# Kernel tuning notes

Measured on AMD Instinct MI355X. Metric: run time of the kernel, lower is better.

The kernel has to match this reference:

```python
import jax, jax.numpy as jnp
import numpy as np

N_CELL, N_GENE, D, E = 100000, 20000, 128, 1000000


def setup_inputs() -> dict:
    key = jax.random.key(0)
    ks = jax.random.split(key, 16)
    return {
        "cell_z": jax.random.normal(ks[0], (N_CELL, D), jnp.float32),
        "gene_z": jax.random.normal(ks[1], (N_GENE, D), jnp.float32),
        "W_gene": jax.random.normal(ks[2], (D, D), jnp.float32) / np.sqrt(D),
        "b_gene": jax.random.normal(ks[3], (D,), jnp.float32) * 0.01,
        "cell_scale": jax.random.normal(ks[4], (N_CELL,), jnp.float32),
        "cell_bias": jax.random.normal(ks[5], (N_CELL,), jnp.float32),
        "cell_std": jax.random.uniform(ks[6], (N_CELL,), jnp.float32, 0.1, 1.0),
        "gene_scale": jax.random.normal(ks[7], (N_GENE,), jnp.float32),
        "gene_bias": jax.random.normal(ks[8], (N_GENE,), jnp.float32),
        "gene_std": jax.random.uniform(ks[9], (N_GENE,), jnp.float32, 0.1, 1.0),
        "src_idx": jax.random.randint(ks[10], (E,), 0, N_CELL, jnp.int32),
        "dst_idx": jax.random.randint(ks[11], (E,), 0, N_GENE, jnp.int32),
        "cell_n_id": jax.random.randint(ks[12], (N_CELL,), 0, N_CELL, jnp.int32),
        "gene_n_id": jax.random.randint(ks[13], (N_GENE,), 0, N_GENE, jnp.int32),
    }


def reference(cell_z, gene_z, W_gene, b_gene,
              cell_scale, cell_bias, cell_std,
              gene_scale, gene_bias, gene_std,
              src_idx, dst_idx, cell_n_id, gene_n_id):
    # Relation projection: 'cell' -> Identity, 'gene' -> Linear + LeakyReLU.
    # Project per-node then gather (mathematically identical to the original
    # gather-then-project since projection is pointwise per node).
    gene_proj = jax.nn.leaky_relu(gene_z @ W_gene + b_gene)  # [N_GENE, D]
    u = cell_z[src_idx]            # [E, D] gather of src node embeddings
    v = gene_proj[dst_idx]         # [E, D] gather of projected dst embeddings

    # Per-edge scale/bias/std lookups via global node ids (n_id[edge_index]).
    sid = cell_n_id[src_idx]       # [E]
    did = gene_n_id[dst_idx]       # [E]
    s_sc, s_b, s_sd = cell_scale[sid], cell_bias[sid], cell_std[sid]
    d_sc, d_b, d_sd = gene_scale[did], gene_bias[did], gene_std[did]

    dot = jnp.sum(u * v, axis=-1)  # [E]
    loc = dot * s_sc * d_sc + s_b + d_b
    std = s_sd * d_sd
    return jnp.stack([loc, std])   # [2, E]
```

## Files before the change

### kernel.cpp

```cpp
#include <hip/hip_runtime.h>

#define N_CELL 100000
#define N_GENE 20000
#define DIM    128
#define N_EDGE 1000000

#define NS_STRIPE 20
#define ND_STRIPE 2
#define NTILE     40
#define NBLK_SORT 977

#define NB_CAST 6250
#define NB_HIST 977
#define NB_PROJ 1250
#define NB_CTAB 391
#define NB_GTAB 79
#define NB_PREP (NB_CAST + NB_HIST + NB_PROJ + NB_CTAB + NB_GTAB)

typedef float f32x4 __attribute__((ext_vector_type(4)));

__device__ inline unsigned short f2bf(float f) {
    unsigned u = __float_as_uint(f);
    u += 0x7fffu + ((u >> 16) & 1u);
    return (unsigned short)(u >> 16);
}

__device__ inline void dot2(float& acc, unsigned a, unsigned b) {
    asm("v_dot2_f32_bf16 %0, %1, %2, %0" : "+v"(acc) : "v"(a), "v"(b));
}

__device__ inline int tile_of(int s, int d) {
    const int ss = (int)(((unsigned long long)s * 429497ULL) >> 31);
    const int ds = (d >= 10000) ? 1 : 0;
    return ds * NS_STRIPE + ss;
}

__device__ inline unsigned pack_sd(int s, int d) {
    return ((unsigned)s << 15) | (unsigned)d;
}

__global__ __launch_bounds__(256) void prep_kernel(
    const float* __restrict__ gene_z,
    const float* __restrict__ W,
    const float* __restrict__ b,
    ushort* __restrict__ gene_projb,
    const float* __restrict__ cell_z,
    ushort4* __restrict__ cell_zb4,
    const int*   __restrict__ src_idx,
    const int*   __restrict__ dst_idx,
    const int*   __restrict__ cell_n_id,
    const int*   __restrict__ gene_n_id,
    const float* __restrict__ cell_scale,
    const float* __restrict__ cell_bias,
    const float* __restrict__ cell_std,
    const float* __restrict__ gene_scale,
    const float* __restrict__ gene_bias,
    const float* __restrict__ gene_std,
    float4* __restrict__ cell_p4,
    float4* __restrict__ gene_p4,
    int* __restrict__ counts)
{
    __shared__ float zlds[16][DIM];

    const int tid = threadIdx.x;
    int blk = blockIdx.x;

    if (blk < NB_CAST) {
        const f32x4* in4 = (const f32x4*)cell_z;
        const int base = blk * 512 + tid;
        const f32x4 v0 = in4[base];
        const f32x4 v1 = in4[base + 256];
        ushort4 o0, o1;
        o0.x = f2bf(v0.x); o0.y = f2bf(v0.y); o0.z = f2bf(v0.z); o0.w = f2bf(v0.w);
        o1.x = f2bf(v1.x); o1.y = f2bf(v1.y); o1.z = f2bf(v1.z); o1.w = f2bf(v1.w);
        cell_zb4[base]       = o0;
        cell_zb4[base + 256] = o1;
        return;
    }
    blk -= NB_CAST;

    if (blk < NB_HIST) {
        if (!counts) return;
        int* lcnt = (int*)&zlds[0][0];
        if (tid < NTILE) lcnt[tid] = 0;
        __syncthreads();
        #pragma unroll
        for (int c = 0; c < 4; ++c) {
            const int e = blk * 1024 + c * 256 + tid;
            if (e < N_EDGE) {
                const int t = tile_of(src_idx[e], dst_idx[e]);
                atomicAdd(&lcnt[t], 1);
            }
        }
        __syncthreads();
        if (tid < NTILE) counts[tid * NBLK_SORT + blk] = lcnt[tid];
        return;
    }
    blk -= NB_HIST;

    if (blk < NB_PROJ) {
        const int row0 = blk * 16;
        const f32x4* Z4  = (const f32x4*)(gene_z + (long)row0 * DIM);
        f32x4*       zl4 = (f32x4*)&zlds[0][0];
        zl4[tid]       = Z4[tid];
        zl4[tid + 256] = Z4[tid + 256];
        __syncthreads();

        const int col   = tid & 127;
        const int rbase = (tid >> 7) * 8;

        const float bias = b[col];
        float acc[8];
        #pragma unroll
        for (int r = 0; r < 8; ++r) acc[r] = bias;

        for (int k4 = 0; k4 < DIM / 4; ++k4) {
            const float w0 = W[(k4 * 4 + 0) * DIM + col];
            const float w1 = W[(k4 * 4 + 1) * DIM + col];
            const float w2 = W[(k4 * 4 + 2) * DIM + col];
            const float w3 = W[(k4 * 4 + 3) * DIM + col];
            #pragma unroll
            for (int rp = 0; rp < 4; ++rp) {
                const float4 za = ((const float4*)&zlds[rbase + 2*rp][0])[k4];
                const float4 zb = ((const float4*)&zlds[rbase + 2*rp + 1][0])[k4];
                acc[2*rp]     = fmaf(za.x, w0, fmaf(za.y, w1,
                                fmaf(za.z, w2, fmaf(za.w, w3, acc[2*rp]))));
                acc[2*rp + 1] = fmaf(zb.x, w0, fmaf(zb.y, w1,
                                fmaf(zb.z, w2, fmaf(zb.w, w3, acc[2*rp + 1]))));
            }
        }
        #pragma unroll
        for (int r = 0; r < 8; ++r) {
            const float v = acc[r];
            gene_projb[(long)(row0 + rbase + r) * DIM + col] =
                f2bf(v > 0.f ? v : 0.01f * v);
        }
        return;
    }
    blk -= NB_PROJ;

    if (blk < NB_CTAB) {
        if (!cell_p4) return;
        const int c = blk * 256 + tid;
        if (c < N_CELL) {
            const int id = cell_n_id[c];
            cell_p4[c] = make_float4(cell_scale[id], cell_bias[id],
                                     cell_std[id], 0.f);
        }
        return;
    }
    blk -= NB_CTAB;

    if (!gene_p4) return;
    const int g = blk * 256 + tid;
    if (g < N_GENE) {
        const int id = gene_n_id[g];
        gene_p4[g] = make_float4(gene_scale[id], gene_bias[id],
                                 gene_std[id], 0.f);
    }
}

__global__ __launch_bounds__(256) void scanA_kernel(
    int* __restrict__ counts, int* __restrict__ totals)
{
    __shared__ int sd[256];
    const int t   = blockIdx.x;
    const int tid = threadIdx.x;
    int carry = 0;
    for (int c = 0; c < 4; ++c) {
        const int idx = c * 256 + tid;
        const int val = (idx < NBLK_SORT) ? counts[t * NBLK_SORT + idx] : 0;
        sd[tid] = val;
        __syncthreads();
        #pragma unroll
        for (int off = 1; off < 256; off <<= 1) {
            const int tmp = (tid >= off) ? sd[tid - off] : 0;
            __syncthreads();
            sd[tid] += tmp;
            __syncthreads();
        }
        const int incl = sd[tid];
        const int ctot = sd[255];
        if (idx < NBLK_SORT) counts[t * NBLK_SORT + idx] = carry + incl - val;
        carry += ctot;
        __syncthreads();
    }
    if (tid == 0) totals[t] = carry;
}

__global__ __launch_bounds__(256) void scatter_kernel(
    const int* __restrict__ src_idx,
    const int* __restrict__ dst_idx,
    const int* __restrict__ counts,
    const int* __restrict__ totals,
    unsigned* __restrict__ sorted_p,
    int*      __restrict__ rank)
{
    __shared__ int lcnt[NTILE];
    __shared__ int sbase[NTILE];
    __shared__ int lbase[NTILE];
    const int tid = threadIdx.x;
    const int blk = blockIdx.x;
    if (tid < NTILE) lcnt[tid] = 0;
    __syncthreads();

    int ts[4], rs[4], ss[4], ds[4];
    #pragma unroll
    for (int c = 0; c < 4; ++c) {
        const int e = blk * 1024 + c * 256 + tid;
        if (e < N_EDGE) {
            ss[c] = src_idx[e];
            ds[c] = dst_idx[e];
            ts[c] = tile_of(ss[c], ds[c]);
            rs[c] = atomicAdd(&lcnt[ts[c]], 1);
        } else { ts[c] = -1; rs[c] = 0; ss[c] = 0; ds[c] = 0; }
    }
    __syncthreads();
    if (tid == 0) {
        int s = 0;
        for (int i = 0; i < NTILE; ++i) { sbase[i] = s; s += totals[i]; }
    }
    __syncthreads();
    if (tid < NTILE) lbase[tid] = sbase[tid] + counts[tid * NBLK_SORT + blk];
    __syncthreads();

    #pragma unroll
    for (int c = 0; c < 4; ++c) {
        const int e = blk * 1024 + c * 256 + tid;
        if (ts[c] >= 0) {
            const int pos = lbase[ts[c]] + rs[c];
            sorted_p[pos] = pack_sd(ss[c], ds[c]);
            rank[e] = pos;
        }
    }
}

__global__ __launch_bounds__(256) void edge_sorted_kernel(
    const ushort* __restrict__ cell_zb,
    const ushort* __restrict__ gene_projb,
    const unsigned* __restrict__ sorted_p,
    const float4* __restrict__ cell_p4,
    const float4* __restrict__ gene_p4,
    float2* __restrict__ res)
{
    const int wg  = blockIdx.x;
    const int xcd = wg & 7;
    const int sub = wg >> 3;
    const int q = 15625 / 8, r = 15625 % 8;
    const int swz = ((xcd < r) ? xcd * (q + 1) : r * (q + 1) + (xcd - r) * q) + sub;

    const int tid  = threadIdx.x;
    const int lane = tid & 15;
    const int grp  = swz * 16 + (tid >> 4);

    const uint4 p = ((const uint4*)sorted_p)[grp];
    const int s0 = (int)(p.x >> 15), d0 = (int)(p.x & 0x7fffu);
    const int s1 = (int)(p.y >> 15), d1 = (int)(p.y & 0x7fffu);
    const int s2 = (int)(p.z >> 15), d2 = (int)(p.z & 0x7fffu);
    const int s3 = (int)(p.w >> 15), d3 = (int)(p.w & 0x7fffu);

    uint4 a0 = ((const uint4*)(cell_zb    + (long)s0 * DIM))[lane];
    uint4 a1 = ((const uint4*)(cell_zb    + (long)s1 * DIM))[lane];
    uint4 a2 = ((const uint4*)(cell_zb    + (long)s2 * DIM))[lane];
    uint4 a3 = ((const uint4*)(cell_zb    + (long)s3 * DIM))[lane];
    uint4 v0 = ((const uint4*)(gene_projb + (long)d0 * DIM))[lane];
    uint4 v1 = ((const uint4*)(gene_projb + (long)d1 * DIM))[lane];
    uint4 v2 = ((const uint4*)(gene_projb + (long)d2 * DIM))[lane];
    uint4 v3 = ((const uint4*)(gene_projb + (long)d3 * DIM))[lane];

    float dot0 = 0.f, dot1 = 0.f, dot2v = 0.f, dot3 = 0.f;
    dot2(dot0, a0.x, v0.x); dot2(dot0, a0.y, v0.y);
    dot2(dot0, a0.z, v0.z); dot2(dot0, a0.w, v0.w);
    dot2(dot1, a1.x, v1.x); dot2(dot1, a1.y, v1.y);
    dot2(dot1, a1.z, v1.z); dot2(dot1, a1.w, v1.w);
    dot2(dot2v, a2.x, v2.x); dot2(dot2v, a2.y, v2.y);
    dot2(dot2v, a2.z, v2.z); dot2(dot2v, a2.w, v2.w);
    dot2(dot3, a3.x, v3.x); dot2(dot3, a3.y, v3.y);
    dot2(dot3, a3.z, v3.z); dot2(dot3, a3.w, v3.w);

    #define RED(d)                 \
        d += __shfl_xor(d, 1);     \
        d += __shfl_xor(d, 2);     \
        d += __shfl_xor(d, 4);     \
        d += __shfl_xor(d, 8);
    RED(dot0) RED(dot1) RED(dot2v) RED(dot3)
    #undef RED

    if (lane < 4) {
        const float dj = (lane & 2) ? ((lane & 1) ? dot3 : dot2v)
                                    : ((lane & 1) ? dot1 : dot0);
        const int sj   = (lane & 2) ? ((lane & 1) ? s3 : s2)
                                    : ((lane & 1) ? s1 : s0);
        const int djx  = (lane & 2) ? ((lane & 1) ? d3 : d2)
                                    : ((lane & 1) ? d1 : d0);
        const float4 cs = cell_p4[sj];
        const float4 gs = gene_p4[djx];
        res[grp * 4 + lane] =
            make_float2(dj * cs.x * gs.x + cs.y + gs.y, cs.z * gs.z);
    }
}

__global__ __launch_bounds__(256) void fixup_kernel(
    const int*    __restrict__ rank,
    const float2* __restrict__ res,
    float* __restrict__ out)
{
    const int e0 = (blockIdx.x * 256 + threadIdx.x) * 4;
    if (e0 >= N_EDGE) return;
    const int4 r4 = *(const int4*)(rank + e0);
    const float2 r0 = res[r4.x];
    const float2 r1 = res[r4.y];
    const float2 r2 = res[r4.z];
    const float2 r3 = res[r4.w];
    *(float4*)(out + e0)          = make_float4(r0.x, r1.x, r2.x, r3.x);
    *(float4*)(out + N_EDGE + e0) = make_float4(r0.y, r1.y, r2.y, r3.y);
}

template<bool TAB>
__global__ __launch_bounds__(256) void edge_kernel(
    const ushort* __restrict__ cell_zb,
    const ushort* __restrict__ gene_projb,
    const int*   __restrict__ src_idx,
    const int*   __restrict__ dst_idx,
    const int*   __restrict__ cell_n_id,
    const int*   __restrict__ gene_n_id,
    const float* __restrict__ cell_scale,
    const float* __restrict__ cell_bias,
    const float* __restrict__ cell_std,
    const float* __restrict__ gene_scale,
    const float* __restrict__ gene_bias,
    const float* __restrict__ gene_std,
    const float4* __restrict__ cell_p4,
    const float4* __restrict__ gene_p4,
    float* __restrict__ out)
{
    const int tid  = threadIdx.x;
    const int lane = tid & 15;
    const int grp  = blockIdx.x * 16 + (tid >> 4);
    const int e0   = grp * 4;

    const int4 s4 = ((const int4*)src_idx)[grp];
    const int4 d4 = ((const int4*)dst_idx)[grp];

    uint4 a0 = ((const uint4*)(cell_zb    + (long)s4.x * DIM))[lane];
    uint4 a1 = ((const uint4*)(cell_zb    + (long)s4.y * DIM))[lane];
    uint4 a2 = ((const uint4*)(cell_zb    + (long)s4.z * DIM))[lane];
    uint4 a3 = ((const uint4*)(cell_zb    + (long)s4.w * DIM))[lane];
    uint4 v0 = ((const uint4*)(gene_projb + (long)d4.x * DIM))[lane];
    uint4 v1 = ((const uint4*)(gene_projb + (long)d4.y * DIM))[lane];
    uint4 v2 = ((const uint4*)(gene_projb + (long)d4.z * DIM))[lane];
    uint4 v3 = ((const uint4*)(gene_projb + (long)d4.w * DIM))[lane];

    float dot0 = 0.f, dot1 = 0.f, dot2v = 0.f, dot3 = 0.f;
    dot2(dot0, a0.x, v0.x); dot2(dot0, a0.y, v0.y);
    dot2(dot0, a0.z, v0.z); dot2(dot0, a0.w, v0.w);
    dot2(dot1, a1.x, v1.x); dot2(dot1, a1.y, v1.y);
    dot2(dot1, a1.z, v1.z); dot2(dot1, a1.w, v1.w);
    dot2(dot2v, a2.x, v2.x); dot2(dot2v, a2.y, v2.y);
    dot2(dot2v, a2.z, v2.z); dot2(dot2v, a2.w, v2.w);
    dot2(dot3, a3.x, v3.x); dot2(dot3, a3.y, v3.y);
    dot2(dot3, a3.z, v3.z); dot2(dot3, a3.w, v3.w);

    #define RED(d)                 \
        d += __shfl_xor(d, 1);     \
        d += __shfl_xor(d, 2);     \
        d += __shfl_xor(d, 4);     \
        d += __shfl_xor(d, 8);
    RED(dot0) RED(dot1) RED(dot2v) RED(dot3)
    #undef RED

    if (lane < 4) {
        const float dj = (lane & 2) ? ((lane & 1) ? dot3 : dot2v)
                                    : ((lane & 1) ? dot1 : dot0);
        const int sj   = (lane & 2) ? ((lane & 1) ? s4.w : s4.z)
                                    : ((lane & 1) ? s4.y : s4.x);
        const int djx  = (lane & 2) ? ((lane & 1) ? d4.w : d4.z)
                                    : ((lane & 1) ? d4.y : d4.x);
        float sc_s, b_s, sd_s, sc_d, b_d, sd_d;
        if (TAB) {
            const float4 cs = cell_p4[sj];
            const float4 gs = gene_p4[djx];
            sc_s = cs.x; b_s = cs.y; sd_s = cs.z;
            sc_d = gs.x; b_d = gs.y; sd_d = gs.z;
        } else {
            const int sid = cell_n_id[sj];
            const int did = gene_n_id[djx];
            sc_s = cell_scale[sid]; b_s = cell_bias[sid]; sd_s = cell_std[sid];
            sc_d = gene_scale[did]; b_d = gene_bias[did]; sd_d = gene_std[did];
        }
        const int e = e0 + lane;
        out[e]          = dj * sc_s * sc_d + b_s + b_d;
        out[N_EDGE + e] = sd_s * sd_d;
    }
}

extern "C" void kernel_launch(void* const* d_in, const int* in_sizes, int n_in,
                              void* d_out, int out_size, void* d_ws, size_t ws_size,
                              hipStream_t stream) {
    const float* cell_z     = (const float*)d_in[0];
    const float* gene_z     = (const float*)d_in[1];
    const float* W_gene     = (const float*)d_in[2];
    const float* b_gene     = (const float*)d_in[3];
    const float* cell_scale = (const float*)d_in[4];
    const float* cell_bias  = (const float*)d_in[5];
    const float* cell_std   = (const float*)d_in[6];
    const float* gene_scale = (const float*)d_in[7];
    const float* gene_bias  = (const float*)d_in[8];
    const float* gene_std   = (const float*)d_in[9];
    const int*   src_idx    = (const int*)d_in[10];
    const int*   dst_idx    = (const int*)d_in[11];
    const int*   cell_n_id  = (const int*)d_in[12];
    const int*   gene_n_id  = (const int*)d_in[13];

    char* ws = (char*)d_ws;
    size_t off = 0;
    ushort* gene_projb = (ushort*)(ws + off); off += (size_t)N_GENE * DIM * 2;
    ushort* cell_zb    = (ushort*)(ws + off); off += (size_t)N_CELL * DIM * 2;
    const size_t base_need = off;

    float4* cell_p4 = nullptr; float4* gene_p4 = nullptr;
    size_t off_tab = off;
    const size_t tab_need = (size_t)N_CELL * 16 + (size_t)N_GENE * 16;

    unsigned* sorted_p = nullptr; int* rank = nullptr; float2* res = nullptr;
    int* counts = nullptr; int* totals = nullptr;
    const size_t sort_need = (size_t)N_EDGE * 4
                           + (size_t)N_EDGE * 4
                           + (size_t)N_EDGE * 8
                           + (size_t)NTILE * NBLK_SORT * 4 + 256;

    const bool tab = (ws_size >= base_need + tab_need);
    const bool srt = tab && (ws_size >= base_need + tab_need + sort_need);

    if (tab) {
        cell_p4 = (float4*)(ws + off_tab);
        gene_p4 = (float4*)(ws + off_tab + (size_t)N_CELL * 16);
        off = off_tab + tab_need;
    }
    if (srt) {
        sorted_p = (unsigned*)(ws + off); off += (size_t)N_EDGE * 4;
        rank     = (int*)(ws + off);      off += (size_t)N_EDGE * 4;
        res      = (float2*)(ws + off);   off += (size_t)N_EDGE * 8;
        counts   = (int*)(ws + off);      off += (size_t)NTILE * NBLK_SORT * 4;
        totals   = (int*)(ws + off);      off += 256;
    }

    float* out = (float*)d_out;

    prep_kernel<<<NB_PREP, 256, 0, stream>>>(
        gene_z, W_gene, b_gene, gene_projb,
        cell_z, (ushort4*)cell_zb,
        src_idx, dst_idx, cell_n_id, gene_n_id,
        cell_scale, cell_bias, cell_std,
        gene_scale, gene_bias, gene_std,
        cell_p4, gene_p4, counts);

    if (srt) {
        scanA_kernel<<<NTILE, 256, 0, stream>>>(counts, totals);
        scatter_kernel<<<NBLK_SORT, 256, 0, stream>>>(
            src_idx, dst_idx, counts, totals, sorted_p, rank);
        edge_sorted_kernel<<<N_EDGE / 64, 256, 0, stream>>>(
            cell_zb, gene_projb, sorted_p, cell_p4, gene_p4, res);
        fixup_kernel<<<(N_EDGE / 4 + 255) / 256, 256, 0, stream>>>(rank, res, out);
    } else if (tab) {
        edge_kernel<true><<<N_EDGE / 64, 256, 0, stream>>>(
            cell_zb, gene_projb, src_idx, dst_idx, cell_n_id, gene_n_id,
            cell_scale, cell_bias, cell_std, gene_scale, gene_bias, gene_std,
            cell_p4, gene_p4, out);
    } else {
        edge_kernel<false><<<N_EDGE / 64, 256, 0, stream>>>(
            cell_zb, gene_projb, src_idx, dst_idx, cell_n_id, gene_n_id,
            cell_scale, cell_bias, cell_std, gene_scale, gene_bias, gene_std,
            nullptr, nullptr, out);
    }
}
```

Before: 87.16 us.

## Convert prep kernel to persistent work-queue with atomic chunk cursor

Replaces the one-block-per-chunk prep launch with 2048 persistent blocks that claim chunks from a global atomic counter. The heavy projection chunks now come first in the order, so the long GEMM work starts early and the cast, histogram and table chunks fill in around it. This targets load imbalance and block-launch overhead. In exchange it adds a memset launch, one global atomic plus a barrier per chunk, and the shared buffers may lower occupancy.

```diff
diff --git a/kernel.cpp b/kernel.cpp
--- a/kernel.cpp
+++ b/kernel.cpp
@@ -6,16 +6,16 @@
 #define N_EDGE 1000000
 
 #define NS_STRIPE 20
-#define ND_STRIPE 2
 #define NTILE     40
 #define NBLK_SORT 977
 
-#define NB_CAST 6250
-#define NB_HIST 977
-#define NB_PROJ 1250
-#define NB_CTAB 391
-#define NB_GTAB 79
-#define NB_PREP (NB_CAST + NB_HIST + NB_PROJ + NB_CTAB + NB_GTAB)
+#define CH_PROJ 1250
+#define CH_HIST 977
+#define CH_CAST 6250
+#define CH_CTAB 391
+#define CH_GTAB 79
+#define CH_TOTAL (CH_PROJ + CH_HIST + CH_CAST + CH_CTAB + CH_GTAB)
+#define NB_WORK 2048
 
 typedef float f32x4 __attribute__((ext_vector_type(4)));
 
@@ -39,7 +39,7 @@
     return ((unsigned)s << 15) | (unsigned)d;
 }
 
-__global__ __launch_bounds__(256) void prep_kernel(
+__global__ __launch_bounds__(256) void work_kernel(
     const float* __restrict__ gene_z,
     const float* __restrict__ W,
     const float* __restrict__ b,
@@ -58,105 +58,113 @@
     const float* __restrict__ gene_std,
     float4* __restrict__ cell_p4,
     float4* __restrict__ gene_p4,
-    int* __restrict__ counts)
+    int* __restrict__ counts,
+    int* __restrict__ cursor)
 {
     __shared__ float zlds[16][DIM];
+    __shared__ int   lcnt[NTILE];
+    __shared__ int   chunk_s;
 
     const int tid = threadIdx.x;
-    int blk = blockIdx.x;
-
-    if (blk < NB_CAST) {
-        const f32x4* in4 = (const f32x4*)cell_z;
-        const int base = blk * 512 + tid;
-        const f32x4 v0 = in4[base];
-        const f32x4 v1 = in4[base + 256];
-        ushort4 o0, o1;
-        o0.x = f2bf(v0.x); o0.y = f2bf(v0.y); o0.z = f2bf(v0.z); o0.w = f2bf(v0.w);
-        o1.x = f2bf(v1.x); o1.y = f2bf(v1.y); o1.z = f2bf(v1.z); o1.w = f2bf(v1.w);
-        cell_zb4[base]       = o0;
-        cell_zb4[base + 256] = o1;
-        return;
-    }
-    blk -= NB_CAST;
-
-    if (blk < NB_HIST) {
-        if (!counts) return;
-        int* lcnt = (int*)&zlds[0][0];
-        if (tid < NTILE) lcnt[tid] = 0;
+
+    for (;;) {
+        if (tid == 0) chunk_s = atomicAdd(cursor, 1);
         __syncthreads();
-        #pragma unroll
-        for (int c = 0; c < 4; ++c) {
-            const int e = blk * 1024 + c * 256 + tid;
-            if (e < N_EDGE) {
-                const int t = tile_of(src_idx[e], dst_idx[e]);
-                atomicAdd(&lcnt[t], 1);
+        int c = chunk_s;
+        if (c >= CH_TOTAL) return;
+
+        if (c < CH_PROJ) {
+            const int row0 = c * 16;
+            const f32x4* Z4  = (const f32x4*)(gene_z + (long)row0 * DIM);
+            f32x4*       zl4 = (f32x4*)&zlds[0][0];
+            zl4[tid]       = Z4[tid];
+            zl4[tid + 256] = Z4[tid + 256];
+            __syncthreads();
+
+            const int col   = tid & 127;
+            const int rbase = (tid >> 7) * 8;
+
+            const float bias = b[col];
+            float acc[8];
+            #pragma unroll
+            for (int r = 0; r < 8; ++r) acc[r] = bias;
+
+            for (int k4 = 0; k4 < DIM / 4; ++k4) {
+                const float w0 = W[(k4 * 4 + 0) * DIM + col];
+                const float w1 = W[(k4 * 4 + 1) * DIM + col];
+                const float w2 = W[(k4 * 4 + 2) * DIM + col];
+                const float w3 = W[(k4 * 4 + 3) * DIM + col];
+                #pragma unroll
+                for (int rp = 0; rp < 4; ++rp) {
+                    const float4 za = ((const float4*)&zlds[rbase + 2*rp][0])[k4];
+                    const float4 zb = ((const float4*)&zlds[rbase + 2*rp + 1][0])[k4];
+                    acc[2*rp]     = fmaf(za.x, w0, fmaf(za.y, w1,
+                                    fmaf(za.z, w2, fmaf(za.w, w3, acc[2*rp]))));
+                    acc[2*rp + 1] = fmaf(zb.x, w0, fmaf(zb.y, w1,
+                                    fmaf(zb.z, w2, fmaf(zb.w, w3, acc[2*rp + 1]))));
+                }
             }
-        }
-        __syncthreads();
-        if (tid < NTILE) counts[tid * NBLK_SORT + blk] = lcnt[tid];
-        return;
-    }
-    blk -= NB_HIST;
-
-    if (blk < NB_PROJ) {
-        const int row0 = blk * 16;
-        const f32x4* Z4  = (const f32x4*)(gene_z + (long)row0 * DIM);
-        f32x4*       zl4 = (f32x4*)&zlds[0][0];
-        zl4[tid]       = Z4[tid];
-        zl4[tid + 256] = Z4[tid + 256];
-        __syncthreads();
-
-        const int col   = tid & 127;
-        const int rbase = (tid >> 7) * 8;
-
-        const float bias = b[col];
-        float acc[8];
-        #pragma unroll
-        for (int r = 0; r < 8; ++r) acc[r] = bias;
-
-        for (int k4 = 0; k4 < DIM / 4; ++k4) {
-            const float w0 = W[(k4 * 4 + 0) * DIM + col];
-            const float w1 = W[(k4 * 4 + 1) * DIM + col];
-            const float w2 = W[(k4 * 4 + 2) * DIM + col];
-            const float w3 = W[(k4 * 4 + 3) * DIM + col];
             #pragma unroll
-            for (int rp = 0; rp < 4; ++rp) {
-                const float4 za = ((const float4*)&zlds[rbase + 2*rp][0])[k4];
-                const float4 zb = ((const float4*)&zlds[rbase + 2*rp + 1][0])[k4];
-                acc[2*rp]     = fmaf(za.x, w0, fmaf(za.y, w1,
-                                fmaf(za.z, w2, fmaf(za.w, w3, acc[2*rp]))));
-                acc[2*rp + 1] = fmaf(zb.x, w0, fmaf(zb.y, w1,
-                                fmaf(zb.z, w2, fmaf(zb.w, w3, acc[2*rp + 1]))));
+            for (int r = 0; r < 8; ++r) {
+                const float v = acc[r];
+                gene_projb[(long)(row0 + rbase + r) * DIM + col] =
+                    f2bf(v > 0.f ? v : 0.01f * v);
             }
-        }
-        #pragma unroll
-        for (int r = 0; r < 8; ++r) {
-            const float v = acc[r];
-            gene_projb[(long)(row0 + rbase + r) * DIM + col] =
-                f2bf(v > 0.f ? v : 0.01f * v);
-        }
-        return;
-    }
-    blk -= NB_PROJ;
-
-    if (blk < NB_CTAB) {
-        if (!cell_p4) return;
-        const int c = blk * 256 + tid;
-        if (c < N_CELL) {
-            const int id = cell_n_id[c];
-            cell_p4[c] = make_float4(cell_scale[id], cell_bias[id],
-                                     cell_std[id], 0.f);
-        }
-        return;
-    }
-    blk -= NB_CTAB;
-
-    if (!gene_p4) return;
-    const int g = blk * 256 + tid;
-    if (g < N_GENE) {
-        const int id = gene_n_id[g];
-        gene_p4[g] = make_float4(gene_scale[id], gene_bias[id],
-                                 gene_std[id], 0.f);
+            continue;
+        }
+        c -= CH_PROJ;
+
+        if (c < CH_HIST) {
+            if (!counts) continue;
+            if (tid < NTILE) lcnt[tid] = 0;
+            __syncthreads();
+            #pragma unroll
+            for (int q = 0; q < 4; ++q) {
+                const int e = c * 1024 + q * 256 + tid;
+                if (e < N_EDGE) {
+                    const int t = tile_of(src_idx[e], dst_idx[e]);
+                    atomicAdd(&lcnt[t], 1);
+                }
+            }
+            __syncthreads();
+            if (tid < NTILE) counts[tid * NBLK_SORT + c] = lcnt[tid];
+            continue;
+        }
+        c -= CH_HIST;
+
+        if (c < CH_CAST) {
+            const f32x4* in4 = (const f32x4*)cell_z;
+            const int base = c * 512 + tid;
+            const f32x4 v0 = in4[base];
+            const f32x4 v1 = in4[base + 256];
+            ushort4 o0, o1;
+            o0.x = f2bf(v0.x); o0.y = f2bf(v0.y); o0.z = f2bf(v0.z); o0.w = f2bf(v0.w);
+            o1.x = f2bf(v1.x); o1.y = f2bf(v1.y); o1.z = f2bf(v1.z); o1.w = f2bf(v1.w);
+            cell_zb4[base]       = o0;
+            cell_zb4[base + 256] = o1;
+            continue;
+        }
+        c -= CH_CAST;
+
+        if (c < CH_CTAB) {
+            if (!cell_p4) continue;
+            const int cc = c * 256 + tid;
+            if (cc < N_CELL) {
+                const int id = cell_n_id[cc];
+                cell_p4[cc] = make_float4(cell_scale[id], cell_bias[id],
+                                          cell_std[id], 0.f);
+            }
+            continue;
+        }
+        c -= CH_CTAB;
+
+        if (!gene_p4) continue;
+        const int g = c * 256 + tid;
+        if (g < N_GENE) {
+            const int id = gene_n_id[g];
+            gene_p4[g] = make_float4(gene_scale[id], gene_bias[id],
+                                     gene_std[id], 0.f);
+        }
     }
 }
 
@@ -416,6 +424,7 @@
     size_t off = 0;
     ushort* gene_projb = (ushort*)(ws + off); off += (size_t)N_GENE * DIM * 2;
     ushort* cell_zb    = (ushort*)(ws + off); off += (size_t)N_CELL * DIM * 2;
+    int*    cursor     = (int*)(ws + off);    off += 256;
     const size_t base_need = off;
 
     float4* cell_p4 = nullptr; float4* gene_p4 = nullptr;
@@ -447,13 +456,14 @@
 
     float* out = (float*)d_out;
 
-    prep_kernel<<<NB_PREP, 256, 0, stream>>>(
+    hipMemsetAsync(cursor, 0, sizeof(int), stream);
+    work_kernel<<<NB_WORK, 256, 0, stream>>>(
         gene_z, W_gene, b_gene, gene_projb,
         cell_z, (ushort4*)cell_zb,
         src_idx, dst_idx, cell_n_id, gene_n_id,
         cell_scale, cell_bias, cell_std,
         gene_scale, gene_bias, gene_std,
-        cell_p4, gene_p4, counts);
+        cell_p4, gene_p4, counts, cursor);
 
     if (srt) {
         scanA_kernel<<<NTILE, 256, 0, stream>>>(counts, totals);
```

Result: slower. 197.7 us (+126.8%).
